# Kernel optimization log

Hardware: AMD Instinct MI355X
Metric: run time of the kernel (lower is better)

## Reference

```python
import jax, jax.numpy as jnp
from jax import lax
import numpy as np

B, CTX, TGT, D_MODEL = 2, 1024, 256, 512
EXPAND, D_STATE, D_CONV, N_LAYERS = 2, 16, 4, 2
D_INNER = EXPAND * D_MODEL
DT_RANK = (D_MODEL + 15) // 16  # 32, mamba_ssm default ceil(d_model/16)
LN_EPS = 1e-5


def setup_inputs() -> dict:
    key = jax.random.key(0)
    ks = jax.random.split(key, 20)
    s = 0.02
    inp = {
        "context_repr": jax.random.normal(ks[0], (B, CTX, D_MODEL), jnp.float32),
        "target_time_emb": jax.random.normal(ks[1], (B, TGT, D_MODEL), jnp.float32),
        "target_var_emb": jax.random.normal(ks[2], (B, TGT, D_MODEL), jnp.float32),
        "target_count": TGT,
        # position_proj / output_proj / LayerNorm params
        "pos_w": jax.random.normal(ks[3], (D_MODEL, 2 * D_MODEL), jnp.float32) * s,
        "pos_b": jnp.zeros((D_MODEL,), jnp.float32),
        "outp_w": jax.random.normal(ks[4], (D_MODEL, D_MODEL), jnp.float32) * s,
        "outp_b": jnp.zeros((D_MODEL,), jnp.float32),
        "ln_g": jnp.ones((D_MODEL,), jnp.float32),
        "ln_b": jnp.zeros((D_MODEL,), jnp.float32),
        # stacked per-layer Mamba params
        "in_w": jax.random.normal(ks[5], (N_LAYERS, 2 * D_INNER, D_MODEL), jnp.float32) * s,
        "conv_w": jax.random.normal(ks[6], (N_LAYERS, D_INNER, D_CONV), jnp.float32) * s,
        "conv_b": jnp.zeros((N_LAYERS, D_INNER), jnp.float32),
        "xproj_w": jax.random.normal(ks[7], (N_LAYERS, DT_RANK + 2 * D_STATE, D_INNER), jnp.float32) * s,
        "dt_w": jax.random.normal(ks[8], (N_LAYERS, D_INNER, DT_RANK), jnp.float32) * s,
        "dt_b": jax.random.normal(ks[9], (N_LAYERS, D_INNER), jnp.float32) * s,
        # A_log init as in mamba_ssm: A = arange(1, d_state+1) repeated over d_inner
        "A_log": jnp.broadcast_to(
            jnp.log(jnp.arange(1, D_STATE + 1, dtype=jnp.float32)),
            (N_LAYERS, D_INNER, D_STATE),
        ).copy(),
        "D_skip": jnp.ones((N_LAYERS, D_INNER), jnp.float32),
        "out_w": jax.random.normal(ks[10], (N_LAYERS, D_MODEL, D_INNER), jnp.float32) * s,
    }
    return inp


def _mamba_block(x, in_w, conv_w, conv_b, xproj_w, dt_w, dt_b, A_log, D_skip, out_w):
    # x: [B, L, d_model]
    Bb, L, _ = x.shape
    xz = jnp.einsum("bld,ed->ble", x, in_w)          # [B, L, 2*d_inner]
    xc, z = jnp.split(xz, 2, axis=-1)
    # causal depthwise conv1d (Conv1d pad=d_conv-1 then [..., :L])
    xt = xc.transpose(0, 2, 1)                        # [B, d_inner, L]
    conv = lax.conv_general_dilated(
        xt, conv_w[:, None, :], (1,), [(D_CONV - 1, 0)],
        feature_group_count=D_INNER,
        dimension_numbers=("NCH", "OIH", "NCH"),
    )
    u = jax.nn.silu(conv + conv_b[None, :, None]).transpose(0, 2, 1)  # [B, L, d_inner]
    x_dbl = jnp.einsum("bld,ed->ble", u, xproj_w)     # [B, L, dt_rank + 2*d_state]
    dt, Bm, Cm = jnp.split(x_dbl, [DT_RANK, DT_RANK + D_STATE], axis=-1)
    delta = jax.nn.softplus(jnp.einsum("blr,dr->bld", dt, dt_w) + dt_b)  # [B, L, d_inner]
    A = -jnp.exp(A_log)                               # [d_inner, d_state]
    dA = jnp.exp(delta[..., None] * A)                # [B, L, d_inner, d_state]
    dBu = delta[..., None] * Bm[:, :, None, :] * u[..., None]

    def step(h, inps):
        dA_t, dBu_t, C_t = inps                       # [B,d_inner,d_state], same, [B,d_state]
        h = dA_t * h + dBu_t
        y = jnp.einsum("bds,bs->bd", h, C_t)
        return h, y

    h0 = jnp.zeros((Bb, D_INNER, D_STATE), x.dtype)
    _, ys = lax.scan(step, h0, (dA.transpose(1, 0, 2, 3), dBu.transpose(1, 0, 2, 3), Cm.transpose(1, 0, 2)))
    y = ys.transpose(1, 0, 2) + u * D_skip            # [B, L, d_inner]
    y = y * jax.nn.silu(z)
    return jnp.einsum("ble,de->bld", y, out_w)        # [B, L, d_model]


def reference(context_repr, target_time_emb, target_var_emb, target_count,
              pos_w, pos_b, outp_w, outp_b, ln_g, ln_b,
              in_w, conv_w, conv_b, xproj_w, dt_w, dt_b, A_log, D_skip, out_w):
    tc = jnp.concatenate([target_time_emb, target_var_emb], axis=-1)      # [B, T, 2*d]
    pos = jnp.einsum("blk,dk->bld", tc, pos_w) + pos_b                    # [B, T, d]
    x = jnp.concatenate([context_repr, pos], axis=1)                      # [B, C+T, d]
    for i in range(N_LAYERS):
        x = x + _mamba_block(x, in_w[i], conv_w[i], conv_b[i], xproj_w[i],
                             dt_w[i], dt_b[i], A_log[i], D_skip[i], out_w[i])
    mu = jnp.mean(x, axis=-1, keepdims=True)
    var = jnp.mean(jnp.square(x - mu), axis=-1, keepdims=True)
    x = (x - mu) * lax.rsqrt(var + LN_EPS) * ln_g + ln_b
    tgt = x[:, -int(target_count):]
    return jnp.einsum("bld,ed->ble", tgt, outp_w) + outp_b
```

## Files before the change

### kernel.cpp

```cpp
#include <hip/hip_runtime.h>
#include <hip/hip_bf16.h>

#define B_     2
#define CTX_   1024
#define TGT_   256
#define DM_    512
#define L_     1280
#define DI_    1024
#define DS_    16
#define DCONV_ 4
#define NL_    2
#define DTR_   32
#define MROWS_ (B_*L_)
#define NC_    80
#define CL_    16
#define XDBL_N_ (MROWS_*64)

typedef unsigned short u16;
typedef __attribute__((ext_vector_type(8))) __bf16 bf16x8;
typedef __attribute__((ext_vector_type(4))) float f32x4;

__device__ __forceinline__ float sigmoidf_(float v){ return 1.f/(1.f+__expf(-v)); }
__device__ __forceinline__ float siluf_(float v){ return v*sigmoidf_(v); }
__device__ __forceinline__ float softplusf_(float v){ return (v>20.f)?v:log1pf(__expf(v)); }
__device__ __forceinline__ u16 f2b(float f){
    union { float f; unsigned u; } x; x.f = f;
    unsigned u = x.u;
    return (u16)((u + 0x7fffu + ((u>>16)&1u)) >> 16);
}
__device__ __forceinline__ float b2f(u16 v){ return __uint_as_float(((unsigned)v)<<16); }
__device__ __forceinline__ void gload_lds16(const void* g, void* l){
    __builtin_amdgcn_global_load_lds((const __attribute__((address_space(1))) unsigned*)g,
                                     (__attribute__((address_space(3))) unsigned*)l, 16, 0, 0);
}
#define PIPE_SYNC do{ asm volatile("s_waitcnt vmcnt(0)" ::: "memory"); \
                      __builtin_amdgcn_sched_barrier(0); \
                      __builtin_amdgcn_s_barrier(); \
                      __builtin_amdgcn_sched_barrier(0); }while(0)

#define G0_ 262144
#define G1_ 131072
#define G2_  65536
#define G3_  32768
#define G4_  16384
__global__ __launch_bounds__(256) void k_init(const float* __restrict__ s0, const float* __restrict__ s1,
                                              const float* __restrict__ s2, const float* __restrict__ s3,
                                              const float* __restrict__ s4,
                                              u16* d0, u16* d1, u16* d2, u16* d3, u16* d4,
                                              const float* __restrict__ ctx, const float* __restrict__ te,
                                              const float* __restrict__ ve, float* __restrict__ x,
                                              u16* __restrict__ xb, u16* __restrict__ tcb){
    int blk = blockIdx.x;
    if (blk < 1984){
        int g = blk*256 + threadIdx.x;
        const float* s; u16* d; int base;
        if      (g < G0_)                { s=s0; d=d0; base=g*8; }
        else if (g < G0_+G1_)            { s=s1; d=d1; base=(g-G0_)*8; }
        else if (g < G0_+G1_+G2_)        { s=s2; d=d2; base=(g-G0_-G1_)*8; }
        else if (g < G0_+G1_+G2_+G3_)    { s=s3; d=d3; base=(g-G0_-G1_-G2_)*8; }
        else                             { s=s4; d=d4; base=(g-G0_-G1_-G2_-G3_)*8; }
        float4 a = *(const float4*)&s[base];
        float4 b = *(const float4*)&s[base+4];
        union { u16 us[8]; uint4 v; } o;
        o.us[0]=f2b(a.x); o.us[1]=f2b(a.y); o.us[2]=f2b(a.z); o.us[3]=f2b(a.w);
        o.us[4]=f2b(b.x); o.us[5]=f2b(b.y); o.us[6]=f2b(b.z); o.us[7]=f2b(b.w);
        *(uint4*)&d[base] = o.v;
    } else if (blk < 1984+1024){
        int e = ((blk-1984)*256 + threadIdx.x)*4;
        int d = e % DM_;
        int l = (e/DM_) % CTX_;
        int b = e/(DM_*CTX_);
        float4 v = *(const float4*)&ctx[e];
        size_t o = ((size_t)(b*L_+l))*DM_ + d;
        *(float4*)&x[o] = v;
        union { u16 us[4]; uint2 q; } p;
        p.us[0]=f2b(v.x); p.us[1]=f2b(v.y); p.us[2]=f2b(v.z); p.us[3]=f2b(v.w);
        *(uint2*)&xb[o] = p.q;
    } else {
        int e = ((blk-1984-1024)*256 + threadIdx.x)*4;
        int k = e % (2*DM_);
        int r = e / (2*DM_);
        float4 v = (k < DM_) ? *(const float4*)&te[(size_t)r*DM_ + k]
                             : *(const float4*)&ve[(size_t)r*DM_ + (k-DM_)];
        union { u16 us[4]; uint2 q; } p;
        p.us[0]=f2b(v.x); p.us[1]=f2b(v.y); p.us[2]=f2b(v.z); p.us[3]=f2b(v.w);
        *(uint2*)&tcb[e] = p.q;
    }
}

template<bool WB>
__global__ __launch_bounds__(512) void k_mmx(const u16* __restrict__ A, int lda,
                                             const u16* __restrict__ Bw, int ldb,
                                             float* __restrict__ C, int ldc,
                                             const float* __restrict__ bias, int K,
                                             u16* __restrict__ Cb, int ldcb){
    __shared__ u16 As[2][128*64];
    __shared__ u16 Bs[2][128*64];
    int tid = threadIdx.x;
    int wave = tid >> 6, lane = tid & 63;
    int bm = blockIdx.y*128, bn = blockIdx.x*128;
    int wr = (wave>>2)*64, wc = (wave&3)*32;
    f32x4 acc[4][2] = {};
    int lrow = lane & 15, lk = (lane>>4)*8;
    int dphys0 = tid*16;
    int dphys1 = dphys0 + 8192;
    int alog0  = dphys0 ^ (((dphys0>>7)&7)<<4);
    int alog1  = dphys1 ^ (((dphys1>>7)&7)<<4);
    int grow0  = alog0 >> 7,         grow1 = alog1 >> 7;
    int gcol0  = (alog0 & 127) >> 1, gcol1 = (alog1 & 127) >> 1;
    const u16* Ar0 = A  + (size_t)(bm+grow0)*lda + gcol0;
    const u16* Ar1 = A  + (size_t)(bm+grow1)*lda + gcol1;
    const u16* Br0 = Bw + (size_t)(bn+grow0)*ldb + gcol0;
    const u16* Br1 = Bw + (size_t)(bn+grow1)*ldb + gcol1;
    int aoff[4][2], boff[2][2];
    #pragma unroll
    for (int f=0; f<4; ++f){
        int ra = wr + f*16 + lrow;
        #pragma unroll
        for (int s=0;s<2;++s) aoff[f][s] = (ra*128 + s*64 + lk*2) ^ ((ra&7)<<4);
    }
    #pragma unroll
    for (int f=0; f<2; ++f){
        int rb = wc + f*16 + lrow;
        #pragma unroll
        for (int s=0;s<2;++s) boff[f][s] = (rb*128 + s*64 + lk*2) ^ ((rb&7)<<4);
    }
    int nt = K >> 6;
    auto stage = [&](int t, int buf){
        int k0 = t*64;
        gload_lds16(Ar0 + k0, &As[buf][wave*512]);
        gload_lds16(Ar1 + k0, &As[buf][4096 + wave*512]);
        gload_lds16(Br0 + k0, &Bs[buf][wave*512]);
        gload_lds16(Br1 + k0, &Bs[buf][4096 + wave*512]);
    };
    stage(0, 0);
    PIPE_SYNC;
    int cur = 0;
    for (int t=0; t<nt; ++t){
        if (t+1 < nt) stage(t+1, cur^1);
        #pragma unroll
        for (int s=0;s<2;++s){
            bf16x8 af[4], bfr[2];
            #pragma unroll
            for (int f=0; f<4; ++f) af[f]  = *(const bf16x8*)((const char*)As[cur] + aoff[f][s]);
            #pragma unroll
            for (int f=0; f<2; ++f) bfr[f] = *(const bf16x8*)((const char*)Bs[cur] + boff[f][s]);
            #pragma unroll
            for (int fm=0; fm<4; ++fm)
                #pragma unroll
                for (int fn=0; fn<2; ++fn)
                    acc[fm][fn] = __builtin_amdgcn_mfma_f32_16x16x32_bf16(af[fm], bfr[fn], acc[fm][fn], 0,0,0);
        }
        PIPE_SYNC;
        cur ^= 1;
    }
    #pragma unroll
    for (int fm=0; fm<4; ++fm){
        int m0 = bm + wr + fm*16 + (lane>>4)*4;
        #pragma unroll
        for (int fn=0; fn<2; ++fn){
            int n = bn + wc + fn*16 + (lane&15);
            float bsv = (!WB && bias) ? bias[n] : 0.f;
            #pragma unroll
            for (int j=0; j<4; ++j){
                float v = acc[fm][fn][j] + bsv;
                if (WB) Cb[(size_t)(m0+j)*ldcb + n] = f2b(v);
                else    C [(size_t)(m0+j)*ldc  + n] = v;
            }
        }
    }
}

template<bool ACC, bool SCAT>
__global__ __launch_bounds__(512) void k_mmx64(const u16* __restrict__ A, int lda,
                                               const u16* __restrict__ Bw, int ldb,
                                               float* __restrict__ C, int ldc,
                                               const float* __restrict__ bias, int ksteps,
                                               u16* __restrict__ Cb, int ldcb){
    __shared__ u16 As[2][64*32];
    __shared__ u16 Bs[2][64*32];
    int tid = threadIdx.x;
    int wave = tid >> 6, lane = tid & 63;
    int bm = blockIdx.y*64;
    int bn = blockIdx.x*64;
    int wr = (wave>>2)*32, wc = (wave&3)*16;
    f32x4 acc[2] = {};
    int lrow = lane & 15, lk = (lane>>4)*8;
    int w4 = wave & 3;
    int dphys = w4*1024 + lane*16;
    int alog  = dphys ^ (((dphys>>7)&7)<<4);
    int grow  = alog >> 6;
    int gcol  = (alog & 63) >> 1;
    bool isB = wave >= 4;
    const u16* Sr = isB ? (Bw + (size_t)(bn+grow)*ldb + gcol)
                        : (A  + (size_t)(bm+grow)*lda + gcol);
    u16* dst0 = isB ? &Bs[0][w4*512] : &As[0][w4*512];
    u16* dst1 = isB ? &Bs[1][w4*512] : &As[1][w4*512];
    int aoff[2], boff;
    #pragma unroll
    for (int f=0; f<2; ++f){
        int ra = wr + f*16 + lrow;
        aoff[f] = (ra*64 + lk*2) ^ (((ra>>1)&7)<<4);
    }
    { int rb = wc + lrow; boff = (rb*64 + lk*2) ^ (((rb>>1)&7)<<4); }
    auto stage = [&](int t, int buf){
        gload_lds16(Sr + t*32, buf ? dst1 : dst0);
    };
    stage(0, 0);
    PIPE_SYNC;
    int cur = 0;
    for (int t = 0; t < ksteps; ++t){
        if (t+1 < ksteps) stage(t+1, cur^1);
        bf16x8 af[2], bfr;
        #pragma unroll
        for (int f=0; f<2; ++f) af[f] = *(const bf16x8*)((const char*)As[cur] + aoff[f]);
        bfr = *(const bf16x8*)((const char*)Bs[cur] + boff);
        #pragma unroll
        for (int fm=0; fm<2; ++fm)
            acc[fm] = __builtin_amdgcn_mfma_f32_16x16x32_bf16(af[fm], bfr, acc[fm], 0,0,0);
        PIPE_SYNC;
        cur ^= 1;
    }
    #pragma unroll
    for (int fm=0; fm<2; ++fm){
        int m0 = bm + wr + fm*16 + (lane>>4)*4;
        int n = bn + wc + (lane&15);
        float bsv = bias ? bias[n] : 0.f;
        #pragma unroll
        for (int j=0; j<4; ++j){
            float v = acc[fm][j] + bsv;
            int m = m0 + j;
            if (SCAT){
                int xrow = (m>>8)*L_ + CTX_ + (m&255);
                C [(size_t)xrow*ldc  + n] = v;
                Cb[(size_t)xrow*ldcb + n] = f2b(v);
            } else {
                size_t off = (size_t)m*ldc + n;
                if (ACC) v += C[off];
                C[off] = v;
                if (Cb) Cb[(size_t)m*ldcb + n] = f2b(v);
            }
        }
    }
}

__global__ __launch_bounds__(512) void k_xproj(const u16* __restrict__ xzb, const u16* __restrict__ Bw,
                                               float* __restrict__ C, const float* __restrict__ cw,
                                               const float* __restrict__ cb){
    __shared__ u16 As[64*32];
    __shared__ u16 Bs[64*32];
    __shared__ u16 sXC[67*32];
    int tid = threadIdx.x;
    int wave = tid >> 6, lane = tid & 63;
    int bm = blockIdx.y*64;
    int kbase = blockIdx.x*128;
    int b0row = (bm/L_)*L_;
    int wr = (wave>>2)*32, wc = (wave&3)*16;
    f32x4 acc[2] = {};
    int lrow = lane & 15, lk = (lane>>4)*8;
    int w4 = wave & 3;
    int dphys = w4*1024 + lane*16;
    int alog  = dphys ^ (((dphys>>7)&7)<<4);
    int grow  = alog >> 6;
    int gcol  = (alog & 63) >> 1;
    const u16* Br = Bw + (size_t)grow*DI_ + gcol;
    int aoff[2], boff;
    #pragma unroll
    for (int f=0; f<2; ++f){
        int ra = wr + f*16 + lrow;
        aoff[f] = (ra*64 + lk*2) ^ (((ra>>1)&7)<<4);
    }
    { int rb = wc + lrow; boff = (rb*64 + lk*2) ^ (((rb>>1)&7)<<4); }
    for (int t = 0; t < 4; ++t){
        int k0 = kbase + t*32;
        if (wave >= 4) gload_lds16(Br + k0, &Bs[w4*512]);
        for (int i = tid; i < 67*32; i += 512){
            int rr = i >> 5, cc = i & 31;
            int gr = bm + rr - 3;
            sXC[i] = (gr >= b0row) ? xzb[(size_t)gr*2048 + k0 + cc] : (u16)0;
        }
        __syncthreads();
        {
            int o = tid*4, rr = o >> 5, cc0 = o & 31;
            union { u16 us[4]; uint2 q; } w;
            #pragma unroll
            for (int j=0;j<4;++j){
                int cc = cc0 + j, d = k0 + cc;
                float4 wv = *(const float4*)&cw[d*4];
                float a = cb[d];
                a = fmaf(b2f(sXC[(rr+0)*32+cc]), wv.x, a);
                a = fmaf(b2f(sXC[(rr+1)*32+cc]), wv.y, a);
                a = fmaf(b2f(sXC[(rr+2)*32+cc]), wv.z, a);
                a = fmaf(b2f(sXC[(rr+3)*32+cc]), wv.w, a);
                w.us[j] = f2b(siluf_(a));
            }
            int L0 = rr*64 + cc0*2;
            int ph = L0 ^ (((L0>>7)&7)<<4);
            *(uint2*)((char*)As + ph) = w.q;
        }
        __syncthreads();
        bf16x8 af[2], bfr;
        #pragma unroll
        for (int f=0; f<2; ++f) af[f] = *(const bf16x8*)((const char*)As + aoff[f]);
        bfr = *(const bf16x8*)((const char*)Bs + boff);
        #pragma unroll
        for (int fm=0; fm<2; ++fm)
            acc[fm] = __builtin_amdgcn_mfma_f32_16x16x32_bf16(af[fm], bfr, acc[fm], 0,0,0);
        __syncthreads();
    }
    float* Cout = C + (size_t)blockIdx.x*XDBL_N_;
    #pragma unroll
    for (int fm=0; fm<2; ++fm){
        int m0 = bm + wr + fm*16 + (lane>>4)*4;
        int n = wc + (lane&15);
        #pragma unroll
        for (int j=0; j<4; ++j)
            Cout[(size_t)(m0+j)*64 + n] = acc[fm][j];
    }
}

__global__ __launch_bounds__(256) void k_scan1(const u16* __restrict__ xzb, const float* __restrict__ xdblp,
                                               const float* __restrict__ dtw, const float* __restrict__ dtb,
                                               const float* __restrict__ cw, const float* __restrict__ cb,
                                               const float* __restrict__ Alog,
                                               float* __restrict__ hend, float* __restrict__ P){
    __shared__ float sX[CL_*64];
    __shared__ float sW[64*33];
    __shared__ float sDtb[64];
    __shared__ float sDel[CL_*64];
    __shared__ float sU[CL_*64];
    __shared__ u16   sXC[19*64];
    int blk = blockIdx.x;
    int dgrp = blk & 15;
    int c = (blk>>4) % NC_;
    int b = blk/(16*NC_);
    int d0 = dgrp*64;
    int tid = threadIdx.x;
    size_t rowbase = (size_t)(b*L_ + c*CL_);
    {
        int e = tid*4;
        float4 s4 = *(const float4*)&xdblp[rowbase*64 + e];
        #pragma unroll
        for (int p=1;p<8;++p){
            float4 t4 = *(const float4*)&xdblp[(size_t)p*XDBL_N_ + rowbase*64 + e];
            s4.x+=t4.x; s4.y+=t4.y; s4.z+=t4.z; s4.w+=t4.w;
        }
        *(float4*)&sX[e] = s4;
        int w0 = tid*8, dr = w0>>5, kk = w0&31;
        float4 wa = *(const float4*)&dtw[(size_t)(d0+dr)*DTR_ + kk];
        float4 wb = *(const float4*)&dtw[(size_t)(d0+dr)*DTR_ + kk + 4];
        sW[dr*33+kk+0]=wa.x; sW[dr*33+kk+1]=wa.y; sW[dr*33+kk+2]=wa.z; sW[dr*33+kk+3]=wa.w;
        sW[dr*33+kk+4]=wb.x; sW[dr*33+kk+5]=wb.y; sW[dr*33+kk+6]=wb.z; sW[dr*33+kk+7]=wb.w;
        if (tid < 64) sDtb[tid] = dtb[d0+tid];
    }
    for (int i = tid; i < 19*64; i += 256){
        int rr = i >> 6, dd = i & 63;
        long gr = (long)rowbase + rr - 3;
        sXC[i] = (gr >= (long)b*L_) ? xzb[(size_t)gr*2048 + d0 + dd] : (u16)0;
    }
    __syncthreads();
    {
        int o = tid*4, t = o>>6, dd0 = o&63;
        #pragma unroll
        for (int j=0;j<4;++j){
            int dd = dd0 + j, d = d0 + dd;
            float4 wv = *(const float4*)&cw[d*4];
            float a = cb[d];
            a = fmaf(b2f(sXC[(t+0)*64+dd]), wv.x, a);
            a = fmaf(b2f(sXC[(t+1)*64+dd]), wv.y, a);
            a = fmaf(b2f(sXC[(t+2)*64+dd]), wv.z, a);
            a = fmaf(b2f(sXC[(t+3)*64+dd]), wv.w, a);
            sU[t*64+dd] = siluf_(a);
        }
    }
    #pragma unroll
    for (int i=0;i<4;++i){
        int idx = tid + i*256;
        int t = idx>>6, dd = idx&63;
        float acc = sDtb[dd];
        #pragma unroll
        for (int k=0;k<DTR_;++k) acc = fmaf(sX[t*64+k], sW[dd*33+k], acc);
        sDel[idx] = softplusf_(acc);
    }
    __syncthreads();
    int dl = tid>>2, sg = (tid&3)*4;
    int d = d0 + dl;
    float A[4];
    #pragma unroll
    for (int i=0;i<4;++i) A[i] = -__expf(Alog[d*DS_ + sg + i]);
    float h[4] = {0,0,0,0}, Pl[4] = {1.f,1.f,1.f,1.f};
    #pragma unroll
    for (int t=0;t<CL_;++t){
        float delta = sDel[t*64+dl];
        float du    = delta*sU[t*64+dl];
        #pragma unroll
        for (int i=0;i<4;++i){
            float a = __expf(delta*A[i]);
            h[i]  = fmaf(a, h[i], du*sX[t*64 + 32 + sg + i]);
            Pl[i] *= a;
        }
    }
    size_t ob = ((size_t)((b*NC_+c)*DI_) + d)*DS_ + sg;
    *(float4*)&hend[ob] = make_float4(h[0],h[1],h[2],h[3]);
    *(float4*)&P[ob]    = make_float4(Pl[0],Pl[1],Pl[2],Pl[3]);
}

__global__ __launch_bounds__(256) void k_scan2(float* __restrict__ hend, const float* __restrict__ P){
    int g = blockIdx.x*256 + threadIdx.x;
    int s = g & 15;
    int d = (g>>4) & 1023;
    int b = g>>14;
    size_t base = ((size_t)b*NC_*DI_ + d)*DS_ + s;
    const size_t cs = (size_t)DI_*DS_;
    float h = 0.f;
    for (int c0=0;c0<NC_;c0+=8){
        float he[8], p[8];
        #pragma unroll
        for (int j=0;j<8;++j){ size_t idx = base + (size_t)(c0+j)*cs; he[j]=hend[idx]; p[j]=P[idx]; }
        #pragma unroll
        for (int j=0;j<8;++j){ size_t idx = base + (size_t)(c0+j)*cs; hend[idx]=h; h=fmaf(p[j],h,he[j]); }
    }
}

__global__ __launch_bounds__(256) void k_scan3(const u16* __restrict__ xzb, const float* __restrict__ xdblp,
                                               const float* __restrict__ dtw, const float* __restrict__ dtb,
                                               const float* __restrict__ cw, const float* __restrict__ cb,
                                               const float* __restrict__ Alog, const float* __restrict__ Dsk,
                                               const float* __restrict__ hstart, u16* __restrict__ yb){
    __shared__ float sX[CL_*64];
    __shared__ float sW[64*33];
    __shared__ float sDtb[64];
    __shared__ float sDel[CL_*64];
    __shared__ float sU[CL_*64];
    __shared__ float sY[CL_*64];
    __shared__ u16   sXC[19*64];
    int blk = blockIdx.x;
    int dgrp = blk & 15;
    int c = (blk>>4) % NC_;
    int b = blk/(16*NC_);
    int d0 = dgrp*64;
    int tid = threadIdx.x;
    size_t rowbase = (size_t)(b*L_ + c*CL_);
    {
        int e = tid*4;
        float4 s4 = *(const float4*)&xdblp[rowbase*64 + e];
        #pragma unroll
        for (int p=1;p<8;++p){
            float4 t4 = *(const float4*)&xdblp[(size_t)p*XDBL_N_ + rowbase*64 + e];
            s4.x+=t4.x; s4.y+=t4.y; s4.z+=t4.z; s4.w+=t4.w;
        }
        *(float4*)&sX[e] = s4;
        int w0 = tid*8, dr = w0>>5, kk = w0&31;
        float4 wa = *(const float4*)&dtw[(size_t)(d0+dr)*DTR_ + kk];
        float4 wb = *(const float4*)&dtw[(size_t)(d0+dr)*DTR_ + kk + 4];
        sW[dr*33+kk+0]=wa.x; sW[dr*33+kk+1]=wa.y; sW[dr*33+kk+2]=wa.z; sW[dr*33+kk+3]=wa.w;
        sW[dr*33+kk+4]=wb.x; sW[dr*33+kk+5]=wb.y; sW[dr*33+kk+6]=wb.z; sW[dr*33+kk+7]=wb.w;
        if (tid < 64) sDtb[tid] = dtb[d0+tid];
    }
    for (int i = tid; i < 19*64; i += 256){
        int rr = i >> 6, dd = i & 63;
        long gr = (long)rowbase + rr - 3;
        sXC[i] = (gr >= (long)b*L_) ? xzb[(size_t)gr*2048 + d0 + dd] : (u16)0;
    }
    __syncthreads();
    {
        int o = tid*4, t = o>>6, dd0 = o&63;
        #pragma unroll
        for (int j=0;j<4;++j){
            int dd = dd0 + j, d = d0 + dd;
            float4 wv = *(const float4*)&cw[d*4];
            float a = cb[d];
            a = fmaf(b2f(sXC[(t+0)*64+dd]), wv.x, a);
            a = fmaf(b2f(sXC[(t+1)*64+dd]), wv.y, a);
            a = fmaf(b2f(sXC[(t+2)*64+dd]), wv.z, a);
            a = fmaf(b2f(sXC[(t+3)*64+dd]), wv.w, a);
            sU[t*64+dd] = siluf_(a);
        }
    }
    #pragma unroll
    for (int i=0;i<4;++i){
        int idx = tid + i*256;
        int t = idx>>6, dd = idx&63;
        float acc = sDtb[dd];
        #pragma unroll
        for (int k=0;k<DTR_;++k) acc = fmaf(sX[t*64+k], sW[dd*33+k], acc);
        sDel[idx] = softplusf_(acc);
    }
    __syncthreads();
    int dl = tid>>2, sg = (tid&3)*4;
    int d = d0 + dl;
    float A[4];
    #pragma unroll
    for (int i=0;i<4;++i) A[i] = -__expf(Alog[d*DS_ + sg + i]);
    size_t ib = ((size_t)((b*NC_+c)*DI_) + d)*DS_ + sg;
    float4 h4 = *(const float4*)&hstart[ib];
    float h[4] = {h4.x, h4.y, h4.z, h4.w};
    #pragma unroll
    for (int t=0;t<CL_;++t){
        float delta = sDel[t*64+dl];
        float du    = delta*sU[t*64+dl];
        float yt = 0.f;
        #pragma unroll
        for (int i=0;i<4;++i){
            float a = __expf(delta*A[i]);
            h[i] = fmaf(a, h[i], du*sX[t*64 + 32 + sg + i]);
            yt   = fmaf(h[i], sX[t*64 + 48 + sg + i], yt);
        }
        yt += __shfl_xor(yt, 1);
        yt += __shfl_xor(yt, 2);
        if ((tid&3)==0) sY[t*64+dl] = yt;
    }
    __syncthreads();
    {
        int e = tid*4, st = e>>6, dd = e&63;
        size_t off = (rowbase+st)*DI_ + d0 + dd;
        float4 dskv = *(const float4*)&Dsk[d0+dd];
        uint2 zz = *(const uint2*)&xzb[(rowbase+st)*2048 + DI_ + d0 + dd];
        float z0 = __uint_as_float(zz.x<<16),  z1 = __uint_as_float(zz.x & 0xffff0000u);
        float z2 = __uint_as_float(zz.y<<16),  z3 = __uint_as_float(zz.y & 0xffff0000u);
        union { u16 us[4]; uint2 q; } o;
        o.us[0] = f2b((sY[e+0] + sU[e+0]*dskv.x) * siluf_(z0));
        o.us[1] = f2b((sY[e+1] + sU[e+1]*dskv.y) * siluf_(z1));
        o.us[2] = f2b((sY[e+2] + sU[e+2]*dskv.z) * siluf_(z2));
        o.us[3] = f2b((sY[e+3] + sU[e+3]*dskv.w) * siluf_(z3));
        *(uint2*)&yb[off] = o.q;
    }
}

__global__ __launch_bounds__(256) void k_ln_tgt(const float* __restrict__ x, const float* __restrict__ g_,
                                                const float* __restrict__ b_, u16* __restrict__ xnb){
    int r = blockIdx.x;
    int b = r / TGT_, t = r % TGT_;
    const float* row = x + ((size_t)(b*L_+CTX_+t))*DM_;
    int tid = threadIdx.x;
    float2 v = *(const float2*)&row[tid*2];
    float s = v.x+v.y, sq = v.x*v.x+v.y*v.y;
    #pragma unroll
    for (int off=32; off; off>>=1){ s += __shfl_down(s,off); sq += __shfl_down(sq,off); }
    __shared__ float ss[4], ssq[4];
    int w = tid>>6, ln = tid&63;
    if (ln==0){ ss[w]=s; ssq[w]=sq; }
    __syncthreads();
    if (tid==0){
        float S=ss[0]+ss[1]+ss[2]+ss[3], Q=ssq[0]+ssq[1]+ssq[2]+ssq[3];
        float mu = S/(float)DM_;
        float var = Q/(float)DM_ - mu*mu;
        ss[0]=mu; ssq[0]=rsqrtf(var+1e-5f);
    }
    __syncthreads();
    float mu=ss[0], rs=ssq[0];
    xnb[(size_t)r*DM_ + tid*2+0] = f2b((v.x-mu)*rs*g_[tid*2+0] + b_[tid*2+0]);
    xnb[(size_t)r*DM_ + tid*2+1] = f2b((v.y-mu)*rs*g_[tid*2+1] + b_[tid*2+1]);
}

extern "C" void kernel_launch(void* const* d_in, const int* in_sizes, int n_in,
                              void* d_out, int out_size, void* d_ws, size_t ws_size,
                              hipStream_t stream) {
    const float* ctx    = (const float*)d_in[0];
    const float* te     = (const float*)d_in[1];
    const float* ve     = (const float*)d_in[2];
    const float* pos_w  = (const float*)d_in[4];
    const float* pos_b  = (const float*)d_in[5];
    const float* outp_w = (const float*)d_in[6];
    const float* outp_b = (const float*)d_in[7];
    const float* ln_g   = (const float*)d_in[8];
    const float* ln_b   = (const float*)d_in[9];
    const float* in_w   = (const float*)d_in[10];
    const float* conv_w = (const float*)d_in[11];
    const float* conv_b = (const float*)d_in[12];
    const float* xproj_w= (const float*)d_in[13];
    const float* dt_w   = (const float*)d_in[14];
    const float* dt_b   = (const float*)d_in[15];
    const float* A_log  = (const float*)d_in[16];
    const float* D_skip = (const float*)d_in[17];
    const float* out_w  = (const float*)d_in[18];
    float* out = (float*)d_out;

    float* ws    = (float*)d_ws;
    float* x     = ws;
    float* hend  = x     + 1310720;
    float* P     = hend  + 2621440;
    float* xdblp = P     + 2621440;
    u16*  xb    = (u16*)(xdblp + 1310720);
    u16*  tcb   = xb    + 1310720;
    u16*  yb    = tcb   + 524288;
    u16*  xnb   = yb    + 2621440;
    u16*  xzb   = xnb   + 262144;
    u16*  inwb  = xzb   + 5242880;
    u16*  outwb = inwb  + 2097152;
    u16*  poswb = outwb + 1048576;
    u16*  outpwb= poswb + 524288;
    u16*  xpwb  = outpwb+ 262144;

    k_init<<<3520, 256, 0, stream>>>(in_w, out_w, pos_w, outp_w, xproj_w,
                                     inwb, outwb, poswb, outpwb, xpwb,
                                     ctx, te, ve, x, xb, tcb);
    k_mmx64<false,true><<<dim3(8,8), 512, 0, stream>>>(tcb, 2*DM_, poswb, 2*DM_, x, DM_, pos_b, 32, xb, DM_);

    for (int i=0;i<NL_;++i){
        const u16*   inwbi  = inwb + (size_t)i*2*DI_*DM_;
        const float* cw     = conv_w  + (size_t)i*DI_*DCONV_;
        const float* cb     = conv_b  + (size_t)i*DI_;
        const u16*   xpwbi  = xpwb + (size_t)i*(DTR_+2*DS_)*DI_;
        const float* dtw    = dt_w    + (size_t)i*DI_*DTR_;
        const float* dtb    = dt_b    + (size_t)i*DI_;
        const float* Ai     = A_log   + (size_t)i*DI_*DS_;
        const float* Dsk    = D_skip  + (size_t)i*DI_;
        const u16*   outwbi = outwb + (size_t)i*DM_*DI_;

        k_mmx<true><<<dim3(16,20), 512, 0, stream>>>(xb, DM_, inwbi, DM_, nullptr, 0, nullptr, DM_, xzb, 2*DI_);
        k_xproj<<<dim3(8,40), 512, 0, stream>>>(xzb, xpwbi, xdblp, cw, cb);
        k_scan1<<<2560, 256, 0, stream>>>(xzb, xdblp, dtw, dtb, cw, cb, Ai, hend, P);
        k_scan2<<<128, 256, 0, stream>>>(hend, P);
        k_scan3<<<2560, 256, 0, stream>>>(xzb, xdblp, dtw, dtb, cw, cb, Ai, Dsk, hend, yb);
        k_mmx64<true,false><<<dim3(8,40), 512, 0, stream>>>(yb, DI_, outwbi, DI_, x, DM_, nullptr, 32, xb, DM_);
    }

    k_ln_tgt<<<512, 256, 0, stream>>>(x, ln_g, ln_b, xnb);
    k_mmx64<false,false><<<dim3(8,8), 512, 0, stream>>>(xnb, DM_, outpwb, DM_, out, DM_, outp_b, 16, nullptr, 0);
}
```

Before: 244.0 us.

## Fuse final LayerNorm into output projection GEMM and vectorize conv-window loads

Replaces the separate target-row LayerNorm kernel and the output GEMM with a single kernel. Each block normalizes its 64 rows into a swizzled LDS tile and then runs a double-buffered MFMA loop over the weight slices, which removes one launch and the round trip of the normalized activations through global memory. Separately, the conv-window staging in the xproj and scan kernels now uses 16-byte vector loads instead of scalar u16 loads. The trade-off is that LayerNorm is recomputed once per column block, eight times per row, and the new kernel needs a 64 KB LDS tile.

```diff
diff --git a/kernel.cpp b/kernel.cpp
--- a/kernel.cpp
+++ b/kernel.cpp
@@ -274,10 +274,12 @@
     for (int t = 0; t < 4; ++t){
         int k0 = kbase + t*32;
         if (wave >= 4) gload_lds16(Br + k0, &Bs[w4*512]);
-        for (int i = tid; i < 67*32; i += 512){
-            int rr = i >> 5, cc = i & 31;
+        if (tid < 268){
+            int rr = tid >> 2, c16 = (tid & 3)*8;
             int gr = bm + rr - 3;
-            sXC[i] = (gr >= b0row) ? xzb[(size_t)gr*2048 + k0 + cc] : (u16)0;
+            uint4 v = make_uint4(0,0,0,0);
+            if (gr >= b0row) v = *(const uint4*)&xzb[(size_t)gr*2048 + k0 + c16];
+            *(uint4*)&sXC[rr*32 + c16] = v;
         }
         __syncthreads();
         {
@@ -353,10 +355,12 @@
         sW[dr*33+kk+4]=wb.x; sW[dr*33+kk+5]=wb.y; sW[dr*33+kk+6]=wb.z; sW[dr*33+kk+7]=wb.w;
         if (tid < 64) sDtb[tid] = dtb[d0+tid];
     }
-    for (int i = tid; i < 19*64; i += 256){
-        int rr = i >> 6, dd = i & 63;
+    if (tid < 152){
+        int rr = tid >> 3, c8 = (tid & 7)*8;
         long gr = (long)rowbase + rr - 3;
-        sXC[i] = (gr >= (long)b*L_) ? xzb[(size_t)gr*2048 + d0 + dd] : (u16)0;
+        uint4 v = make_uint4(0,0,0,0);
+        if (gr >= (long)b*L_) v = *(const uint4*)&xzb[(size_t)gr*2048 + d0 + c8];
+        *(uint4*)&sXC[rr*64 + c8] = v;
     }
     __syncthreads();
     {
@@ -457,10 +461,12 @@
         sW[dr*33+kk+4]=wb.x; sW[dr*33+kk+5]=wb.y; sW[dr*33+kk+6]=wb.z; sW[dr*33+kk+7]=wb.w;
         if (tid < 64) sDtb[tid] = dtb[d0+tid];
     }
-    for (int i = tid; i < 19*64; i += 256){
-        int rr = i >> 6, dd = i & 63;
+    if (tid < 152){
+        int rr = tid >> 3, c8 = (tid & 7)*8;
         long gr = (long)rowbase + rr - 3;
-        sXC[i] = (gr >= (long)b*L_) ? xzb[(size_t)gr*2048 + d0 + dd] : (u16)0;
+        uint4 v = make_uint4(0,0,0,0);
+        if (gr >= (long)b*L_) v = *(const uint4*)&xzb[(size_t)gr*2048 + d0 + c8];
+        *(uint4*)&sXC[rr*64 + c8] = v;
     }
     __syncthreads();
     {
@@ -527,30 +533,75 @@
     }
 }
 
-__global__ __launch_bounds__(256) void k_ln_tgt(const float* __restrict__ x, const float* __restrict__ g_,
-                                                const float* __restrict__ b_, u16* __restrict__ xnb){
-    int r = blockIdx.x;
-    int b = r / TGT_, t = r % TGT_;
-    const float* row = x + ((size_t)(b*L_+CTX_+t))*DM_;
+__global__ __launch_bounds__(512) void k_lnmm(const float* __restrict__ x, const float* __restrict__ g_,
+                                              const float* __restrict__ be_,
+                                              const u16* __restrict__ Bw,
+                                              const float* __restrict__ bias, float* __restrict__ out){
+    __shared__ u16 ALn[64*512];
+    __shared__ u16 Bs[2][64*32];
     int tid = threadIdx.x;
-    float2 v = *(const float2*)&row[tid*2];
-    float s = v.x+v.y, sq = v.x*v.x+v.y*v.y;
-    #pragma unroll
-    for (int off=32; off; off>>=1){ s += __shfl_down(s,off); sq += __shfl_down(sq,off); }
-    __shared__ float ss[4], ssq[4];
-    int w = tid>>6, ln = tid&63;
-    if (ln==0){ ss[w]=s; ssq[w]=sq; }
+    int wave = tid >> 6, lane = tid & 63;
+    int bm = blockIdx.y*64, bn = blockIdx.x*64;
+    for (int rr8 = 0; rr8 < 8; ++rr8){
+        int rr = wave*8 + rr8;
+        int tr = bm + rr;
+        int xrow = (tr>>8)*L_ + CTX_ + (tr&255);
+        const float* row = x + (size_t)xrow*DM_ + lane*8;
+        float4 a = *(const float4*)row;
+        float4 b = *(const float4*)(row+4);
+        float s  = a.x+a.y+a.z+a.w + b.x+b.y+b.z+b.w;
+        float sq = a.x*a.x+a.y*a.y+a.z*a.z+a.w*a.w + b.x*b.x+b.y*b.y+b.z*b.z+b.w*b.w;
+        #pragma unroll
+        for (int off=32; off; off>>=1){ s += __shfl_xor(s,off); sq += __shfl_xor(sq,off); }
+        float mu = s*(1.f/DM_);
+        float rs = rsqrtf(sq*(1.f/DM_) - mu*mu + 1e-5f);
+        int c0 = lane*8;
+        float4 g0 = *(const float4*)&g_[c0],  g1 = *(const float4*)&g_[c0+4];
+        float4 b0 = *(const float4*)&be_[c0], b1 = *(const float4*)&be_[c0+4];
+        union { u16 us[8]; uint4 v; } o;
+        o.us[0]=f2b((a.x-mu)*rs*g0.x+b0.x); o.us[1]=f2b((a.y-mu)*rs*g0.y+b0.y);
+        o.us[2]=f2b((a.z-mu)*rs*g0.z+b0.z); o.us[3]=f2b((a.w-mu)*rs*g0.w+b0.w);
+        o.us[4]=f2b((b.x-mu)*rs*g1.x+b1.x); o.us[5]=f2b((b.y-mu)*rs*g1.y+b1.y);
+        o.us[6]=f2b((b.z-mu)*rs*g1.z+b1.z); o.us[7]=f2b((b.w-mu)*rs*g1.w+b1.w);
+        int ph = (rr*1024) + ((lane*16) ^ ((rr&7)<<4));
+        *(uint4*)((char*)ALn + ph) = o.v;
+    }
     __syncthreads();
-    if (tid==0){
-        float S=ss[0]+ss[1]+ss[2]+ss[3], Q=ssq[0]+ssq[1]+ssq[2]+ssq[3];
-        float mu = S/(float)DM_;
-        float var = Q/(float)DM_ - mu*mu;
-        ss[0]=mu; ssq[0]=rsqrtf(var+1e-5f);
-    }
-    __syncthreads();
-    float mu=ss[0], rs=ssq[0];
-    xnb[(size_t)r*DM_ + tid*2+0] = f2b((v.x-mu)*rs*g_[tid*2+0] + b_[tid*2+0]);
-    xnb[(size_t)r*DM_ + tid*2+1] = f2b((v.y-mu)*rs*g_[tid*2+1] + b_[tid*2+1]);
+    int wr = (wave>>2)*32, wc = (wave&3)*16;
+    f32x4 acc[2] = {};
+    int lrow = lane & 15, lk = (lane>>4)*8;
+    int w4 = wave & 3;
+    int dphys = w4*1024 + lane*16;
+    int alog  = dphys ^ (((dphys>>7)&7)<<4);
+    int grow  = alog >> 6;
+    int gcol  = (alog & 63) >> 1;
+    const u16* Sr = Bw + (size_t)(bn+grow)*DM_ + gcol;
+    int boff;
+    { int rb = wc + lrow; boff = (rb*64 + lk*2) ^ (((rb>>1)&7)<<4); }
+    int ra0 = wr + lrow, ra1 = wr + 16 + lrow;
+    if (wave >= 4) gload_lds16(Sr, &Bs[0][w4*512]);
+    PIPE_SYNC;
+    int cur = 0;
+    for (int t = 0; t < 16; ++t){
+        if (t+1 < 16 && wave >= 4) gload_lds16(Sr + (t+1)*32, &Bs[cur^1][w4*512]);
+        int kb = (t*32 + lk)*2;
+        bf16x8 af0 = *(const bf16x8*)((const char*)ALn + (ra0*1024 + (kb ^ ((ra0&7)<<4))));
+        bf16x8 af1 = *(const bf16x8*)((const char*)ALn + (ra1*1024 + (kb ^ ((ra1&7)<<4))));
+        bf16x8 bfr = *(const bf16x8*)((const char*)Bs[cur] + boff);
+        acc[0] = __builtin_amdgcn_mfma_f32_16x16x32_bf16(af0, bfr, acc[0], 0,0,0);
+        acc[1] = __builtin_amdgcn_mfma_f32_16x16x32_bf16(af1, bfr, acc[1], 0,0,0);
+        PIPE_SYNC;
+        cur ^= 1;
+    }
+    #pragma unroll
+    for (int fm=0; fm<2; ++fm){
+        int m0 = bm + wr + fm*16 + (lane>>4)*4;
+        int n = bn + wc + (lane&15);
+        float bsv = bias[n];
+        #pragma unroll
+        for (int j=0; j<4; ++j)
+            out[(size_t)(m0+j)*DM_ + n] = acc[fm][j] + bsv;
+    }
 }
 
 extern "C" void kernel_launch(void* const* d_in, const int* in_sizes, int n_in,
@@ -584,8 +635,7 @@
     u16*  xb    = (u16*)(xdblp + 1310720);
     u16*  tcb   = xb    + 1310720;
     u16*  yb    = tcb   + 524288;
-    u16*  xnb   = yb    + 2621440;
-    u16*  xzb   = xnb   + 262144;
+    u16*  xzb   = yb    + 2621440;
     u16*  inwb  = xzb   + 5242880;
     u16*  outwb = inwb  + 2097152;
     u16*  poswb = outwb + 1048576;
@@ -616,6 +666,5 @@
         k_mmx64<true,false><<<dim3(8,40), 512, 0, stream>>>(yb, DI_, outwbi, DI_, x, DM_, nullptr, 32, xb, DM_);
     }
 
-    k_ln_tgt<<<512, 256, 0, stream>>>(x, ln_g, ln_b, xnb);
-    k_mmx64<false,false><<<dim3(8,8), 512, 0, stream>>>(xnb, DM_, outpwb, DM_, out, DM_, outp_b, 16, nullptr, 0);
-}
+    k_lnmm<<<dim3(8,8), 512, 0, stream>>>(x, ln_g, ln_b, outpwb, outp_b, out);
+}
```

New measurement: 228.9 us. -6.2%, faster.
